# Kernel tuning notes

Hardware: AMD Instinct MI355X
Metric: run time of the kernel (lower is better)

Reference implementation:

```python
import jax, jax.numpy as jnp
import numpy as np

CONF_THRESHOLD = 4.0
NMS_THRESHOLD = 0.5
TOP_K = 4096        # fixed candidate cap for jit-static shapes (>> expected #candidates)
NEG = -1.0e9


def setup_inputs() -> dict:
    key = jax.random.key(0)
    k1, k2, k3 = jax.random.split(key, 3)
    B, N, C = 8, 65536, 80
    logits = jax.random.normal(k1, (B, N, C), dtype=jnp.float32)
    # valid xyxy boxes in a ~1000px image: x2>x1, y2>y1
    xy = jax.random.uniform(k2, (B, N, 2), dtype=jnp.float32) * 900.0
    wh = jax.random.uniform(k3, (B, N, 2), dtype=jnp.float32) * 100.0 + 1.0
    boxes = jnp.concatenate([xy, xy + wh], axis=-1)
    return {"logits": logits, "boxes": boxes}


def _pairwise_iou(b):
    # b: [K, 4] xyxy -> [K, K] IoU (torchvision convention, no +1)
    x1, y1, x2, y2 = b[:, 0], b[:, 1], b[:, 2], b[:, 3]
    area = (x2 - x1) * (y2 - y1)                      # [K]
    iw = jnp.maximum(jnp.minimum(x2[:, None], x2[None, :]) - jnp.maximum(x1[:, None], x1[None, :]), 0.0)
    ih = jnp.maximum(jnp.minimum(y2[:, None], y2[None, :]) - jnp.maximum(y1[:, None], y1[None, :]), 0.0)
    inter = iw * ih                                   # [K, K]
    union = area[:, None] + area[None, :] - inter
    return inter / jnp.maximum(union, 1e-12)


def reference(logits, boxes):
    B, N, C = logits.shape
    scores = jnp.max(logits, axis=2)                  # [B, N]
    cls = jnp.argmax(logits, axis=2)                  # [B, N]
    # per-(image, class) NMS category id, as in the torch module
    cat = cls + jnp.arange(B, dtype=cls.dtype)[:, None] * C
    valid = scores > CONF_THRESHOLD                   # [B, N]
    img = jnp.broadcast_to(jnp.arange(B, dtype=jnp.int32)[:, None], (B, N))

    scores_f = scores.reshape(-1)
    valid_f = valid.reshape(-1)
    boxes_f = boxes.reshape(-1, 4)
    cat_f = cat.reshape(-1)
    cls_f = cls.reshape(-1)
    img_f = img.reshape(-1)

    # global descending-score order (matches batched_nms sort); invalid pushed to bottom
    vals, idx = jax.lax.top_k(jnp.where(valid_f, scores_f, NEG), TOP_K)
    bx = boxes_f[idx]                                 # [K, 4]
    ct = cat_f[idx]
    cl = cls_f[idx]
    im = img_f[idx]
    vk = valid_f[idx]                                 # [K]

    iou = _pairwise_iou(bx)                           # [K, K]
    suppress_mat = (ct[:, None] == ct[None, :]) & (iou > NMS_THRESHOLD)
    order = jnp.arange(TOP_K)

    def body(i, keep):
        sup = suppress_mat[i] & (order > i)
        return jnp.where(keep[i], keep & ~sup, keep)

    keep = jax.lax.fori_loop(0, TOP_K, body, vk)      # greedy NMS suppression

    nms_image_idx = jnp.where(keep, im, -1)
    nms_bboxes = bx * keep[:, None].astype(bx.dtype)
    nms_classes = jnp.where(keep, cl, -1)
    nms_scores = jnp.where(keep, vals, 0.0)
    return (nms_image_idx, nms_bboxes, nms_classes, nms_scores)
```

## Files before the change

### kernel.cpp

```cpp
#include <hip/hip_runtime.h>
#include <stdint.h>

typedef unsigned long long u64;
typedef unsigned int u32;

#define BATCH  8
#define NPTS   65536
#define NCLS   80
#define NANCH  (BATCH * NPTS)
#define TOPK   4096
#define CONF   4.0f
#define NMSTH  0.5f
#define NCAT   (BATCH * NCLS)
#define BCAP   32

static constexpr size_t OFF_CNT    = 0;
static constexpr size_t OFF_KEYS   = 64;
static constexpr size_t OFF_SORTED = OFF_KEYS + 8192 * 8;

__global__ __launch_bounds__(64) void k_score(const float* __restrict__ logits,
                                              int* __restrict__ cnt,
                                              u64* __restrict__ keys) {
    __shared__ u64 red[64 * 21];
    int lane = threadIdx.x;
    const float4* src = (const float4*)logits + (size_t)blockIdx.x * 1280;
#pragma unroll
    for (int k = 0; k < 20; ++k) {
        int e = k * 64 + lane;
        float4 v = src[e];
        float bv = v.x; int bc = 0;
        if (v.y > bv) { bv = v.y; bc = 1; }
        if (v.z > bv) { bv = v.z; bc = 2; }
        if (v.w > bv) { bv = v.w; bc = 3; }
        int a_l = e / 20;
        int j   = e % 20;
        int cls = j * 4 + bc;
        u32 eb = __float_as_uint(bv);
        eb = (eb & 0x80000000u) ? ~eb : (eb | 0x80000000u);
        red[a_l * 21 + j] = ((u64)eb << 32) | (u32)(255 - cls);
    }
    __syncthreads();
    u64 best = 0;
#pragma unroll
    for (int j = 0; j < 20; ++j) {
        u64 p = red[lane * 21 + j];
        best = (p > best) ? p : best;
    }
    u32 eb = (u32)(best >> 32);
    u32 orig = (eb & 0x80000000u) ? (eb & 0x7fffffffu) : ~eb;
    float sc = __uint_as_float(orig);
    if (sc > CONF) {
        int pos = atomicAdd(cnt, 1);
        if (pos < 8192) {
            u32 cls = 255u - (u32)(best & 0xffu);
            u32 a = blockIdx.x * 64 + lane;
            u64 low = (((~a) & 0x7FFFFu) << 7) | cls;
            keys[pos] = ((u64)eb << 32) | low;
        }
    }
}

__global__ __launch_bounds__(1024) void k_sort(const int* __restrict__ cnt,
                                               const u64* __restrict__ keys_raw,
                                               u64* __restrict__ keys_sorted) {
    __shared__ u64 sk[4096];
    int n = min(*cnt, 4096);
    int n2 = 64; while (n2 < n) n2 <<= 1;
    for (int i = threadIdx.x; i < n2; i += 1024)
        sk[i] = (i < n) ? keys_raw[i] : 0ull;
    __syncthreads();
    for (int k = 2; k <= n2; k <<= 1) {
        for (int j = k >> 1; j > 0; j >>= 1) {
            for (int i = threadIdx.x; i < n2; i += 1024) {
                int ixj = i ^ j;
                if (ixj > i) {
                    u64 x = sk[i], y = sk[ixj];
                    bool desc = ((i & k) == 0);
                    if (desc ? (x < y) : (x > y)) { sk[i] = y; sk[ixj] = x; }
                }
            }
            __syncthreads();
        }
    }
    for (int i = threadIdx.x; i < n2; i += 1024)
        keys_sorted[i] = sk[i];
}

__global__ __launch_bounds__(1024) void k_nms(const int* __restrict__ cnt,
                                              const u64* __restrict__ keys_sorted,
                                              const float* __restrict__ boxes,
                                              float* __restrict__ out) {
    __shared__ float4 s_box[4096];
    __shared__ unsigned short s_bucket[NCAT * BCAP];
    __shared__ int s_bcnt[NCAT];
    __shared__ unsigned char s_keep[4096];
    int n = min(*cnt, TOPK);
    int tid = threadIdx.x;

    for (int c = tid; c < NCAT; c += 1024) s_bcnt[c] = 0;

    float4 bx[4]; int cls_[4], img_[4]; float sc_[4];
#pragma unroll
    for (int r = 0; r < 4; ++r) {
        int s = tid + 1024 * r;
        float4 b = make_float4(0.f, 0.f, 0.f, 0.f);
        int cl = -1, im = -1; float v = 0.f;
        if (s < n) {
            u64 key = keys_sorted[s];
            u32 eb = (u32)(key >> 32);
            u32 orig = (eb & 0x80000000u) ? (eb & 0x7fffffffu) : ~eb;
            v = __uint_as_float(orig);
            u32 low = (u32)key;
            cl = (int)(low & 0x7fu);
            u32 a = (~(low >> 7)) & 0x7FFFFu;
            im = (int)(a >> 16);
            b = ((const float4*)boxes)[a];
        }
        bx[r] = b; cls_[r] = cl; img_[r] = im; sc_[r] = v;
        s_box[s]  = b;
        s_keep[s] = (s < n) ? 1 : 0;
    }
    __syncthreads();

#pragma unroll
    for (int r = 0; r < 4; ++r) {
        int s = tid + 1024 * r;
        if (s < n) {
            int c = img_[r] * NCLS + cls_[r];
            int pos = atomicAdd(&s_bcnt[c], 1);
            if (pos < BCAP) s_bucket[c * BCAP + pos] = (unsigned short)s;
        }
    }
    __syncthreads();

    if (tid < NCAT) {
        int m = min(s_bcnt[tid], BCAP);
        unsigned short* bkt = &s_bucket[tid * BCAP];
        if (m > 1) {
            for (int i = 1; i < m; ++i) {
                unsigned short x = bkt[i]; int j = i - 1;
                while (j >= 0 && bkt[j] > x) { bkt[j + 1] = bkt[j]; --j; }
                bkt[j + 1] = x;
            }
            for (int i = 1; i < m; ++i) {
                float4 bi = s_box[bkt[i]];
                float areai = (bi.z - bi.x) * (bi.w - bi.y);
                bool dead = false;
                for (int j = 0; j < i && !dead; ++j) {
                    if (!s_keep[bkt[j]]) continue;
                    float4 bj = s_box[bkt[j]];
                    float iw = fmaxf(fminf(bi.z, bj.z) - fmaxf(bi.x, bj.x), 0.f);
                    float ih = fmaxf(fminf(bi.w, bj.w) - fmaxf(bi.y, bj.y), 0.f);
                    float inter = iw * ih;
                    float uni = areai + (bj.z - bj.x) * (bj.w - bj.y) - inter;
                    if (inter / fmaxf(uni, 1e-12f) > NMSTH) dead = true;
                }
                if (dead) s_keep[bkt[i]] = 0;
            }
        }
    }
    __syncthreads();

#pragma unroll
    for (int r = 0; r < 4; ++r) {
        int s = tid + 1024 * r;
        bool keep = s_keep[s] != 0;
        out[s] = keep ? (float)img_[r] : -1.0f;
        ((float4*)(out + 4096))[s] = keep ? bx[r] : make_float4(0.f, 0.f, 0.f, 0.f);
        out[4096 + 16384 + s]        = keep ? (float)cls_[r] : -1.0f;
        out[4096 + 16384 + 4096 + s] = keep ? sc_[r] : 0.0f;
    }
}

extern "C" void kernel_launch(void* const* d_in, const int* in_sizes, int n_in,
                              void* d_out, int out_size, void* d_ws, size_t ws_size,
                              hipStream_t stream) {
    const float* logits = (const float*)d_in[0];
    const float* boxes  = (const float*)d_in[1];
    float* out = (float*)d_out;
    char* ws = (char*)d_ws;

    int* cnt         = (int*)(ws + OFF_CNT);
    u64* keys_raw    = (u64*)(ws + OFF_KEYS);
    u64* keys_sorted = (u64*)(ws + OFF_SORTED);

    hipMemsetAsync(cnt, 0, 64, stream);
    k_score<<<NANCH / 64, 64, 0, stream>>>(logits, cnt, keys_raw);
    k_sort<<<1, 1024, 0, stream>>>(cnt, keys_raw, keys_sorted);
    k_nms<<<1, 1024, 0, stream>>>(cnt, keys_sorted, boxes, out);
}
```

Baseline: 281.9 us.

## Fuse sort into NMS kernel, shrink score reduction LDS, use nontemporal loads

Merges the bitonic sort into the NMS kernel so sorted keys stay in LDS, removing one kernel launch and a global round trip. Also merges the bucket-insert loop into the decode loop, dropping one barrier. The score kernel now stores 32-bit scores plus byte class ids instead of 64-bit packed keys, and reads logits with nontemporal loads. The NMS kernel now needs more LDS (an extra 32KB), which is fine for a single block.

```diff
diff --git a/kernel.cpp b/kernel.cpp
--- a/kernel.cpp
+++ b/kernel.cpp
@@ -3,6 +3,7 @@
 
 typedef unsigned long long u64;
 typedef unsigned int u32;
+typedef float fv4 __attribute__((ext_vector_type(4)));
 
 #define BATCH  8
 #define NPTS   65536
@@ -14,90 +15,78 @@
 #define NCAT   (BATCH * NCLS)
 #define BCAP   32
 
-static constexpr size_t OFF_CNT    = 0;
-static constexpr size_t OFF_KEYS   = 64;
-static constexpr size_t OFF_SORTED = OFF_KEYS + 8192 * 8;
+static constexpr size_t OFF_CNT  = 0;
+static constexpr size_t OFF_KEYS = 64;
 
 __global__ __launch_bounds__(64) void k_score(const float* __restrict__ logits,
                                               int* __restrict__ cnt,
                                               u64* __restrict__ keys) {
-    __shared__ u64 red[64 * 21];
+    __shared__ u32 s_sc[64 * 21];
+    __shared__ unsigned char s_cl[64 * 20];
     int lane = threadIdx.x;
-    const float4* src = (const float4*)logits + (size_t)blockIdx.x * 1280;
+    const fv4* src = (const fv4*)logits + (size_t)blockIdx.x * 1280;
 #pragma unroll
     for (int k = 0; k < 20; ++k) {
         int e = k * 64 + lane;
-        float4 v = src[e];
+        fv4 v = __builtin_nontemporal_load(&src[e]);
         float bv = v.x; int bc = 0;
         if (v.y > bv) { bv = v.y; bc = 1; }
         if (v.z > bv) { bv = v.z; bc = 2; }
         if (v.w > bv) { bv = v.w; bc = 3; }
-        int a_l = e / 20;
-        int j   = e % 20;
-        int cls = j * 4 + bc;
+        int a_l = e / 20, j = e % 20;
         u32 eb = __float_as_uint(bv);
         eb = (eb & 0x80000000u) ? ~eb : (eb | 0x80000000u);
-        red[a_l * 21 + j] = ((u64)eb << 32) | (u32)(255 - cls);
+        s_sc[a_l * 21 + j] = eb;
+        s_cl[a_l * 20 + j] = (unsigned char)(j * 4 + bc);
     }
     __syncthreads();
-    u64 best = 0;
+    u32 best = 0; int bj = 0;
 #pragma unroll
     for (int j = 0; j < 20; ++j) {
-        u64 p = red[lane * 21 + j];
-        best = (p > best) ? p : best;
+        u32 p = s_sc[lane * 21 + j];
+        if (p > best) { best = p; bj = j; }
     }
-    u32 eb = (u32)(best >> 32);
-    u32 orig = (eb & 0x80000000u) ? (eb & 0x7fffffffu) : ~eb;
-    float sc = __uint_as_float(orig);
-    if (sc > CONF) {
+    u32 orig = (best & 0x80000000u) ? (best & 0x7fffffffu) : ~best;
+    if (__uint_as_float(orig) > CONF) {
+        u32 cls = s_cl[lane * 20 + bj];
+        u32 a = blockIdx.x * 64 + (u32)lane;
         int pos = atomicAdd(cnt, 1);
-        if (pos < 8192) {
-            u32 cls = 255u - (u32)(best & 0xffu);
-            u32 a = blockIdx.x * 64 + lane;
-            u64 low = (((~a) & 0x7FFFFu) << 7) | cls;
-            keys[pos] = ((u64)eb << 32) | low;
-        }
+        if (pos < 8192)
+            keys[pos] = ((u64)best << 32) | ((((~a) & 0x7FFFFu) << 7) | cls);
     }
 }
 
-__global__ __launch_bounds__(1024) void k_sort(const int* __restrict__ cnt,
-                                               const u64* __restrict__ keys_raw,
-                                               u64* __restrict__ keys_sorted) {
-    __shared__ u64 sk[4096];
-    int n = min(*cnt, 4096);
-    int n2 = 64; while (n2 < n) n2 <<= 1;
-    for (int i = threadIdx.x; i < n2; i += 1024)
-        sk[i] = (i < n) ? keys_raw[i] : 0ull;
-    __syncthreads();
-    for (int k = 2; k <= n2; k <<= 1) {
-        for (int j = k >> 1; j > 0; j >>= 1) {
-            for (int i = threadIdx.x; i < n2; i += 1024) {
-                int ixj = i ^ j;
-                if (ixj > i) {
-                    u64 x = sk[i], y = sk[ixj];
-                    bool desc = ((i & k) == 0);
-                    if (desc ? (x < y) : (x > y)) { sk[i] = y; sk[ixj] = x; }
-                }
-            }
-            __syncthreads();
-        }
-    }
-    for (int i = threadIdx.x; i < n2; i += 1024)
-        keys_sorted[i] = sk[i];
-}
-
 __global__ __launch_bounds__(1024) void k_nms(const int* __restrict__ cnt,
-                                              const u64* __restrict__ keys_sorted,
+                                              const u64* __restrict__ keys_raw,
                                               const float* __restrict__ boxes,
                                               float* __restrict__ out) {
+    __shared__ u64    s_keys[4096];
     __shared__ float4 s_box[4096];
     __shared__ unsigned short s_bucket[NCAT * BCAP];
     __shared__ int s_bcnt[NCAT];
     __shared__ unsigned char s_keep[4096];
     int n = min(*cnt, TOPK);
     int tid = threadIdx.x;
+    int n2 = 64; while (n2 < n) n2 <<= 1;
 
     for (int c = tid; c < NCAT; c += 1024) s_bcnt[c] = 0;
+    for (int i = tid; i < n2; i += 1024)
+        s_keys[i] = (i < n) ? keys_raw[i] : 0ull;
+    __syncthreads();
+
+    for (int k = 2; k <= n2; k <<= 1) {
+        for (int j = k >> 1; j > 0; j >>= 1) {
+            for (int i = tid; i < n2; i += 1024) {
+                int ixj = i ^ j;
+                if (ixj > i) {
+                    u64 x = s_keys[i], y = s_keys[ixj];
+                    bool desc = ((i & k) == 0);
+                    if (desc ? (x < y) : (x > y)) { s_keys[i] = y; s_keys[ixj] = x; }
+                }
+            }
+            __syncthreads();
+        }
+    }
 
     float4 bx[4]; int cls_[4], img_[4]; float sc_[4];
 #pragma unroll
@@ -106,7 +95,7 @@
         float4 b = make_float4(0.f, 0.f, 0.f, 0.f);
         int cl = -1, im = -1; float v = 0.f;
         if (s < n) {
-            u64 key = keys_sorted[s];
+            u64 key = s_keys[s];
             u32 eb = (u32)(key >> 32);
             u32 orig = (eb & 0x80000000u) ? (eb & 0x7fffffffu) : ~eb;
             v = __uint_as_float(orig);
@@ -115,21 +104,13 @@
             u32 a = (~(low >> 7)) & 0x7FFFFu;
             im = (int)(a >> 16);
             b = ((const float4*)boxes)[a];
+            int c = im * NCLS + cl;
+            int pos = atomicAdd(&s_bcnt[c], 1);
+            if (pos < BCAP) s_bucket[c * BCAP + pos] = (unsigned short)s;
         }
         bx[r] = b; cls_[r] = cl; img_[r] = im; sc_[r] = v;
         s_box[s]  = b;
         s_keep[s] = (s < n) ? 1 : 0;
-    }
-    __syncthreads();
-
-#pragma unroll
-    for (int r = 0; r < 4; ++r) {
-        int s = tid + 1024 * r;
-        if (s < n) {
-            int c = img_[r] * NCLS + cls_[r];
-            int pos = atomicAdd(&s_bcnt[c], 1);
-            if (pos < BCAP) s_bucket[c * BCAP + pos] = (unsigned short)s;
-        }
     }
     __syncthreads();
 
@@ -180,12 +161,10 @@
     float* out = (float*)d_out;
     char* ws = (char*)d_ws;
 
-    int* cnt         = (int*)(ws + OFF_CNT);
-    u64* keys_raw    = (u64*)(ws + OFF_KEYS);
-    u64* keys_sorted = (u64*)(ws + OFF_SORTED);
+    int* cnt      = (int*)(ws + OFF_CNT);
+    u64* keys_raw = (u64*)(ws + OFF_KEYS);
 
     hipMemsetAsync(cnt, 0, 64, stream);
     k_score<<<NANCH / 64, 64, 0, stream>>>(logits, cnt, keys_raw);
-    k_sort<<<1, 1024, 0, stream>>>(cnt, keys_raw, keys_sorted);
-    k_nms<<<1, 1024, 0, stream>>>(cnt, keys_sorted, boxes, out);
+    k_nms<<<1, 1024, 0, stream>>>(cnt, keys_raw, boxes, out);
 }
```

New measurement: 269.2 us. 1.05x faster.
